# Kernel optimization log

Measured on AMD Instinct MI355X. Metric: run time of the kernel, lower is better.

Reference implementation:

```python
import jax, jax.numpy as jnp
import numpy as np
import math

N = 100000
E = 1600000
D_IN = 128
H = 128
OUT = 10
NEG = -1e30


def setup_inputs() -> dict:
    key = jax.random.key(0)
    ks = jax.random.split(key, 24)
    def lin(k, fi, fo):
        s = 1.0 / np.sqrt(fi)
        return jax.random.uniform(k, (fi, fo), jnp.float32, -s, s)
    inp = {
        'x': jax.random.normal(ks[0], (N, D_IN), jnp.float32),
        'edge_index': jax.random.randint(ks[1], (2, E), 0, N, jnp.int64),
        'W1': lin(ks[2], D_IN, H), 'b1': jnp.zeros((H,), jnp.float32),
        'ws1': lin(ks[3], H, 1), 'bs1': jnp.zeros((1,), jnp.float32),
        'W2': lin(ks[4], H, H), 'b2': jnp.zeros((H,), jnp.float32),
        'ws2': lin(ks[5], H, 1), 'bs2': jnp.zeros((1,), jnp.float32),
        'W3': lin(ks[6], H, H), 'b3': jnp.zeros((H,), jnp.float32),
        'ws3': lin(ks[7], H, 1), 'bs3': jnp.zeros((1,), jnp.float32),
        'M1': lin(ks[8], 2 * H, H), 'bm1': jnp.zeros((H,), jnp.float32),
        'M2': lin(ks[9], H, H // 2), 'bm2': jnp.zeros((H // 2,), jnp.float32),
        'M3': lin(ks[10], H // 2, OUT), 'bm3': jnp.zeros((OUT,), jnp.float32),
    }
    return inp


def _gcn(x, W, b, src, dst, node_mask, edge_mask):
    # GCNConv with self-loops: deg[i] = self_loop + in_degree over valid edges
    deg = node_mask + jax.ops.segment_sum(edge_mask, dst, num_segments=N)
    dinv = jnp.where(deg > 0, jax.lax.rsqrt(deg), 0.0)
    coef = edge_mask * dinv[src] * dinv[dst]            # [E]
    agg = jax.ops.segment_sum(coef[:, None] * x[src], dst, num_segments=N)
    agg = agg + (node_mask * dinv * dinv)[:, None] * x   # self-loop term
    return (agg @ W + b) * node_mask[:, None]


def _sag_pool(x, ws, bs, src, dst, node_mask, edge_mask, k):
    # score via 1-dim GCNConv, top-k (ratio 0.5) select, tanh gating, edge filtering
    score = _gcn(x, ws, bs, src, dst, node_mask, edge_mask)[:, 0]
    _, idx = jax.lax.top_k(jnp.where(node_mask > 0, score, -jnp.inf), k)
    new_mask = jnp.zeros((N,), x.dtype).at[idx].set(1.0)
    x_new = x * jnp.tanh(score)[:, None] * new_mask[:, None]
    e_new = edge_mask * new_mask[src] * new_mask[dst]
    return x_new, new_mask, e_new


def _readout(x, mask, k):
    mean = jnp.sum(x * mask[:, None], axis=0) / k
    mx = jnp.max(jnp.where(mask[:, None] > 0, x, NEG), axis=0)
    return jnp.concatenate([mean, mx])[None, :]   # [1, 2H]


def reference(x, edge_index, W1, b1, ws1, bs1, W2, b2, ws2, bs2, W3, b3, ws3, bs3, M1, bm1, M2, bm2, M3, bm3):
    src, dst = edge_index[0], edge_index[1]
    nm0 = jnp.ones((N,), jnp.float32)
    em0 = jnp.ones((E,), jnp.float32)
    k1 = math.ceil(0.5 * N)
    k2 = math.ceil(0.5 * k1)
    k3 = math.ceil(0.5 * k2)

    h1 = jax.nn.relu(_gcn(x, W1, b1, src, dst, nm0, em0))
    x1, nm1, em1 = _sag_pool(h1, ws1, bs1, src, dst, nm0, em0, k1)
    r1 = _readout(x1, nm1, k1)

    h2 = jax.nn.relu(_gcn(x1, W2, b2, src, dst, nm1, em1))
    x2, nm2, em2 = _sag_pool(h2, ws2, bs2, src, dst, nm1, em1, k2)
    r2 = _readout(x2, nm2, k2)

    h3 = jax.nn.relu(_gcn(x2, W3, b3, src, dst, nm2, em2))
    x3, nm3, em3 = _sag_pool(h3, ws3, bs3, src, dst, nm2, em2, k3)
    r3 = _readout(x3, nm3, k3)

    readout = r1 + r2 + r3                              # [1, 2H]
    y = jax.nn.relu(readout @ M1 + bm1)
    y = jax.nn.relu(y @ M2 + bm2)
    y = y @ M3 + bm3
    return jax.nn.log_softmax(y, axis=1)
```

## Files before the change

### kernel.cpp

```cpp
#include <hip/hip_runtime.h>
#include <cstdint>
#include <cstddef>

#define NN 100000
#define EE 1600000
#define HH 128
#define NB_N 391
#define NBKT 391
#define CAP 5120
#define NCH 16
#define SPC 25


typedef float f32x2 __attribute__((ext_vector_type(2)));
typedef float f32x4 __attribute__((ext_vector_type(4)));
typedef short bf16x8 __attribute__((ext_vector_type(8)));

static __device__ __forceinline__ unsigned fsort_(float f){
  unsigned u = __float_as_uint(f);
  return (u & 0x80000000u) ? ~u : (u | 0x80000000u);
}
static __device__ __forceinline__ unsigned bfbits_(float f){
  unsigned u = __float_as_uint(f);
  return (u + 0x7FFFu + ((u >> 16) & 1u)) >> 16;
}
static __device__ __forceinline__ unsigned bfpack_(float f0, float f1){
  return bfbits_(f0) | (bfbits_(f1) << 16);
}
static __device__ __forceinline__ float bflo_(unsigned u){ return __uint_as_float(u << 16); }
static __device__ __forceinline__ float bfhi_(unsigned u){ return __uint_as_float(u & 0xFFFF0000u); }

__global__ void k_init(const int* __restrict__ ei, unsigned* __restrict__ state,
                       unsigned* __restrict__ bktcnt,
                       const float* __restrict__ W0, const float* __restrict__ W1,
                       const float* __restrict__ W2,
                       unsigned short* __restrict__ WtH, unsigned short* __restrict__ WtL){
  int t = threadIdx.x;
  if(blockIdx.x == 3){
    if(t < 64){
      int v = ei[2*t + 1];
      unsigned long long m = __ballot(v != 0);
      if(t == 0) state[8] = (m == 0ull) ? 1u : 0u;
    }
    if(t >= 12 && t < 24) state[t] = 0u;
    for(int j=t; j<NBKT; j+=256) bktcnt[j] = 0u;
  } else {
    int m = blockIdx.x;
    const float* W = (m==0)?W0:((m==1)?W1:W2);
    unsigned short* th = WtH + m*16384;
    unsigned short* tl = WtL + m*16384;
    for(int i=t; i<16384; i+=256){
      int k = i & 127, n = i >> 7;
      float w = W[k*128 + n];
      unsigned hb = bfbits_(w);
      float hf = __uint_as_float(hb<<16);
      unsigned lb = bfbits_(w - hf);
      th[n*128 + k] = (unsigned short)hb;
      tl[n*128 + k] = (unsigned short)lb;
    }
  }
}

__global__ __launch_bounds__(256) void k_binA(const int* __restrict__ ei,
                     const unsigned* __restrict__ state,
                     unsigned* __restrict__ bktcnt, unsigned* __restrict__ staging){
  __shared__ unsigned lcnt[NBKT];
  __shared__ unsigned gbase[NBKT];
  __shared__ unsigned lloc[NBKT];
  __shared__ unsigned pfx[512];
  __shared__ unsigned sortv[4096];
  __shared__ unsigned short bktid[4096];
  int t = threadIdx.x;
  for(int j=t; j<NBKT; j+=256){ lcnt[j] = 0u; lloc[j] = 0u; }
  bool i64 = (state[8] != 0u);
  int e0 = blockIdx.x*4096;
  int es[16], ed[16];
  #pragma unroll
  for(int k=0;k<16;k++){
    int e = e0 + k*256 + t;
    int s = -1, d = 0;
    if(e < EE){
      if(i64){ s = ei[2*e]; d = ei[2*EE + 2*e]; }
      else   { s = ei[e];   d = ei[EE + e]; }
    }
    es[k] = s; ed[k] = d;
  }
  __syncthreads();
  #pragma unroll
  for(int k=0;k<16;k++){
    if(es[k] >= 0) atomicAdd(&lcnt[ed[k]>>8], 1u);
  }
  __syncthreads();
  int j0 = t, j1 = t + 256;
  pfx[j0] = (j0 < NBKT) ? lcnt[j0] : 0u;
  pfx[j1] = (j1 < NBKT) ? lcnt[j1] : 0u;
  __syncthreads();
  for(int off=1; off<512; off<<=1){
    unsigned u0 = (j0 >= off) ? pfx[j0-off] : 0u;
    unsigned u1 = (j1 >= off) ? pfx[j1-off] : 0u;
    __syncthreads();
    pfx[j0] += u0;
    pfx[j1] += u1;
    __syncthreads();
  }
  unsigned total = pfx[NBKT-1];
  for(int j=t; j<NBKT; j+=256){
    unsigned c = lcnt[j];
    gbase[j] = c ? atomicAdd(&bktcnt[j], c) : 0u;
  }
  __syncthreads();
  #pragma unroll
  for(int k=0;k<16;k++){
    if(es[k] >= 0){
      int b = ed[k] >> 8;
      unsigned slot = (pfx[b] - lcnt[b]) + atomicAdd(&lloc[b], 1u);
      sortv[slot] = (unsigned)es[k] | (((unsigned)(ed[k] & 255)) << 17);
      bktid[slot] = (unsigned short)b;
    }
  }
  __syncthreads();
  for(unsigned i=t; i<total; i+=256){
    unsigned b = bktid[i];
    unsigned local = i - (pfx[b] - lcnt[b]);
    unsigned off = gbase[b] + local;
    if(off < CAP) staging[b*CAP + off] = sortv[i];
  }
}

__global__ __launch_bounds__(256) void k_binB(const unsigned* __restrict__ staging,
                     const unsigned* __restrict__ bktcnt,
                     int* __restrict__ rs, int* __restrict__ rl, int* __restrict__ col,
                     float* __restrict__ dinv){
  __shared__ unsigned hist[256];
  __shared__ unsigned pref[256];
  __shared__ unsigned lfill[256];
  __shared__ unsigned baseSh;
  __shared__ int colsh[CAP];
  int t = threadIdx.x;
  int b = blockIdx.x;
  unsigned s = 0;
  for(int j=t; j<b; j+=256) s += bktcnt[j];
  pref[t] = s;
  __syncthreads();
  for(int off=128; off>0; off>>=1){
    if(t < off) pref[t] += pref[t+off];
    __syncthreads();
  }
  if(t == 0) baseSh = pref[0];
  __syncthreads();
  unsigned base = baseSh;
  unsigned cnt = bktcnt[b]; if(cnt > CAP) cnt = CAP;
  hist[t] = 0u; lfill[t] = 0u;
  __syncthreads();
  const unsigned* st = staging + (unsigned)b*CAP;
  for(unsigned i=t; i<cnt; i+=256) atomicAdd(&hist[st[i]>>17], 1u);
  __syncthreads();
  unsigned h = hist[t];
  pref[t] = h;
  __syncthreads();
  for(int off=1; off<256; off<<=1){
    unsigned u = (t >= off) ? pref[t-off] : 0u;
    __syncthreads();
    pref[t] += u;
    __syncthreads();
  }
  unsigned excl = pref[t] - h;
  int node = b*256 + t;
  if(node < NN){
    rs[node] = (int)(base + excl);
    rl[node] = (int)h;
    dinv[node] = rsqrtf(1.f + (float)h);
  }
  __syncthreads();
  pref[t] = excl;
  __syncthreads();
  for(unsigned i=t; i<cnt; i+=256){
    unsigned w = st[i];
    unsigned dl = w >> 17;
    unsigned pos = pref[dl] + atomicAdd(&lfill[dl], 1u);
    colsh[pos] = (int)(w & 0x1FFFFu);
  }
  __syncthreads();
  for(unsigned i=t; i<cnt; i+=256) col[base+i] = colsh[i];
}

template<int MODE>
__global__ __launch_bounds__(256) void k_gemmM(const void* __restrict__ xin_,
        const float* __restrict__ gate, const float* __restrict__ dinv,
        const int* __restrict__ alist, int nrows,
        const unsigned short* __restrict__ WtH, const unsigned short* __restrict__ WtL,
        unsigned short* __restrict__ y16){
  __shared__ __attribute__((aligned(16))) unsigned short sWh[128*128];
  __shared__ __attribute__((aligned(16))) unsigned short sWl[128*128];
  __shared__ __attribute__((aligned(16))) unsigned short sB[4][16*128];
  int t = threadIdx.x;
  for(int f = t; f < 2048; f += 256){
    int colw = f >> 4, kc = f & 15;
    uint4 vh = *(const uint4*)(WtH + colw*128 + kc*8);
    uint4 vl = *(const uint4*)(WtL + colw*128 + kc*8);
    int dst = colw*128 + ((kc ^ (colw & 15)) << 3);
    *(uint4*)&sWh[dst] = vh;
    *(uint4*)&sWl[dst] = vl;
  }
  int lane = t & 63, wid = t >> 6;
  int lg = lane >> 4, lc = lane & 15;
  int rb = blockIdx.x*64 + wid*16;
  int arow = rb + lc;
  int anode = 0;
  if(arow < nrows) anode = MODE ? alist[arow] : arow;
  bf16x8 a_h[4], a_l[4];
  if(MODE){
    const unsigned short* xp = (const unsigned short*)xin_ + (size_t)anode*HH + lg*8;
    #pragma unroll
    for(int kw=0;kw<4;kw++) a_h[kw] = *(const bf16x8*)(xp + kw*32);
  } else {
    const float* xp = (const float*)xin_ + (size_t)anode*HH + lg*8;
    #pragma unroll
    for(int kw=0;kw<4;kw++){
      float4 x0 = *(const float4*)(xp + kw*32);
      float4 x1 = *(const float4*)(xp + kw*32 + 4);
      float xs[8] = {x0.x,x0.y,x0.z,x0.w,x1.x,x1.y,x1.z,x1.w};
      #pragma unroll
      for(int e=0;e<8;e++){
        unsigned hb = bfbits_(xs[e]);
        float hf = __uint_as_float(hb<<16);
        unsigned lb = bfbits_(xs[e]-hf);
        a_h[kw][e] = (short)hb;
        a_l[kw][e] = (short)lb;
      }
    }
  }
  __syncthreads();
  f32x4 acc[8];
  #pragma unroll
  for(int c=0;c<8;c++) acc[c] = (f32x4){0.f,0.f,0.f,0.f};
  #pragma unroll
  for(int kw=0;kw<4;kw++){
    int kch = kw*4 + lg;
    bf16x8 bh[8], bl[8];
    #pragma unroll
    for(int c=0;c<8;c++){
      int idx = (c*16 + lc)*128 + ((kch ^ lc) << 3);
      bh[c] = *(const bf16x8*)&sWh[idx];
      bl[c] = *(const bf16x8*)&sWl[idx];
    }
    #pragma unroll
    for(int c=0;c<8;c++)
      acc[c] = __builtin_amdgcn_mfma_f32_16x16x32_bf16(a_h[kw], bh[c], acc[c], 0,0,0);
    if(MODE){
      #pragma unroll
      for(int c=0;c<8;c++)
        acc[c] = __builtin_amdgcn_mfma_f32_16x16x32_bf16(a_h[kw], bl[c], acc[c], 0,0,0);
    } else {
      #pragma unroll
      for(int c=0;c<8;c++)
        acc[c] = __builtin_amdgcn_mfma_f32_16x16x32_bf16(a_l[kw], bh[c], acc[c], 0,0,0);
      #pragma unroll
      for(int c=0;c<8;c++)
        acc[c] = __builtin_amdgcn_mfma_f32_16x16x32_bf16(a_h[kw], bl[c], acc[c], 0,0,0);
    }
  }
  float s[4];
  #pragma unroll
  for(int r=0;r<4;r++){
    int gr = rb + lg*4 + r;
    float sv = 0.f;
    if(gr < nrows){
      int nd = MODE ? alist[gr] : gr;
      sv = MODE ? dinv[nd]*gate[nd] : dinv[nd];
    }
    s[r] = sv;
  }
  #pragma unroll
  for(int c=0;c<8;c++){
    #pragma unroll
    for(int r=0;r<4;r++)
      sB[wid][(lg*4+r)*128 + c*16 + lc] = (unsigned short)bfbits_(acc[c][r]*s[r]);
  }
  #pragma unroll
  for(int it=0; it<4; it++){
    int row = it*4 + lg;
    int grow = rb + row;
    uint4 v = *(const uint4*)&sB[wid][row*128 + lc*8];
    if(grow < nrows){
      int nd = MODE ? alist[grow] : grow;
      *(uint4*)&y16[(size_t)nd*HH + lc*8] = v;
    }
  }
}

#define ACCQ(V) do{ \
  f32x2 t0,t1,t2,t3; \
  t0.x=__uint_as_float((V).x<<16); t0.y=__uint_as_float((V).x&0xFFFF0000u); \
  t1.x=__uint_as_float((V).y<<16); t1.y=__uint_as_float((V).y&0xFFFF0000u); \
  t2.x=__uint_as_float((V).z<<16); t2.y=__uint_as_float((V).z&0xFFFF0000u); \
  t3.x=__uint_as_float((V).w<<16); t3.y=__uint_as_float((V).w&0xFFFF0000u); \
  a01+=t0; a23+=t1; a45+=t2; a67+=t3; }while(0)

template<int LIST>
__global__ __launch_bounds__(256) void k_agg(const unsigned short* __restrict__ y16,
        const float* __restrict__ dinv,
        const int* __restrict__ rs, const int* __restrict__ rl,
        const int* __restrict__ col, const int* __restrict__ alist,
        const float* __restrict__ bias, const float* __restrict__ wsc,
        unsigned short* __restrict__ h16, float* __restrict__ p,
        unsigned* __restrict__ hist){
  if(blockIdx.x < 512) hist[blockIdx.x*256 + threadIdx.x] = 0u;
  int w = (blockIdx.x*256 + threadIdx.x) >> 6;
  int lane = threadIdx.x & 63;
  int g = lane >> 4, c = lane & 15;
  int node = LIST ? alist[w] : w;
  float di = dinv[node];
  int e0 = rs[node], len = rl[node];
  const char* yb = (const char*)y16;
  unsigned lc16 = (unsigned)(c << 4);
  int chunk = (len + 3) >> 2;
  int ib = g*chunk;
  int ie = ib + chunk; if(ie > len) ie = len;
  f32x2 a01 = {0.f,0.f}, a23 = {0.f,0.f}, a45 = {0.f,0.f}, a67 = {0.f,0.f};
  const int* ce = col + e0;
  int i = ib;
  for(; i+3 < ie; i += 4){
    int c0 = ce[i], c1 = ce[i+1], c2 = ce[i+2], c3 = ce[i+3];
    uint4 v0 = *(const uint4*)(yb + (((unsigned)c0<<8) | lc16));
    uint4 v1 = *(const uint4*)(yb + (((unsigned)c1<<8) | lc16));
    uint4 v2 = *(const uint4*)(yb + (((unsigned)c2<<8) | lc16));
    uint4 v3 = *(const uint4*)(yb + (((unsigned)c3<<8) | lc16));
    ACCQ(v0); ACCQ(v1); ACCQ(v2); ACCQ(v3);
  }
  for(; i < ie; i++){
    int c0 = ce[i];
    uint4 v0 = *(const uint4*)(yb + (((unsigned)c0<<8) | lc16));
    ACCQ(v0);
  }
  float a0=a01.x, a1=a01.y, a2=a23.x, a3=a23.y, a4=a45.x, a5=a45.y, a6=a67.x, a7=a67.y;
  a0 += __shfl_xor(a0,16,64); a0 += __shfl_xor(a0,32,64);
  a1 += __shfl_xor(a1,16,64); a1 += __shfl_xor(a1,32,64);
  a2 += __shfl_xor(a2,16,64); a2 += __shfl_xor(a2,32,64);
  a3 += __shfl_xor(a3,16,64); a3 += __shfl_xor(a3,32,64);
  a4 += __shfl_xor(a4,16,64); a4 += __shfl_xor(a4,32,64);
  a5 += __shfl_xor(a5,16,64); a5 += __shfl_xor(a5,32,64);
  a6 += __shfl_xor(a6,16,64); a6 += __shfl_xor(a6,32,64);
  a7 += __shfl_xor(a7,16,64); a7 += __shfl_xor(a7,32,64);
  uint4 sv = *(const uint4*)(yb + (((unsigned)node<<8) | lc16));
  const float4* b4 = (const float4*)bias;
  float4 bb0 = b4[2*c], bb1 = b4[2*c+1];
  float o0 = fmaxf(fmaf(di, a0 + bflo_(sv.x), bb0.x), 0.f);
  float o1 = fmaxf(fmaf(di, a1 + bfhi_(sv.x), bb0.y), 0.f);
  float o2 = fmaxf(fmaf(di, a2 + bflo_(sv.y), bb0.z), 0.f);
  float o3 = fmaxf(fmaf(di, a3 + bfhi_(sv.y), bb0.w), 0.f);
  float o4 = fmaxf(fmaf(di, a4 + bflo_(sv.z), bb1.x), 0.f);
  float o5 = fmaxf(fmaf(di, a5 + bfhi_(sv.z), bb1.y), 0.f);
  float o6 = fmaxf(fmaf(di, a6 + bflo_(sv.w), bb1.z), 0.f);
  float o7 = fmaxf(fmaf(di, a7 + bfhi_(sv.w), bb1.w), 0.f);
  if(g == 0){
    uint4 o;
    o.x = bfpack_(o0,o1); o.y = bfpack_(o2,o3);
    o.z = bfpack_(o4,o5); o.w = bfpack_(o6,o7);
    ((uint4*)(h16 + (size_t)node*HH))[c] = o;
  }
  const float4* w4 = (const float4*)wsc;
  float4 w0 = w4[2*c], w1 = w4[2*c+1];
  float pp = o0*w0.x + o1*w0.y + o2*w0.z + o3*w0.w
           + o4*w1.x + o5*w1.y + o6*w1.z + o7*w1.w;
  pp += __shfl_xor(pp, 1, 64);
  pp += __shfl_xor(pp, 2, 64);
  pp += __shfl_xor(pp, 4, 64);
  pp += __shfl_xor(pp, 8, 64);
  if(lane == 0) p[node] = di*pp;
}

template<int LIST>
__global__ void k_score(const float* __restrict__ p, const float* __restrict__ dinv,
                        const int* __restrict__ rs, const int* __restrict__ rl,
                        const int* __restrict__ col, const int* __restrict__ alist, int n,
                        const float* __restrict__ bs, float* __restrict__ score,
                        unsigned* __restrict__ key, unsigned* __restrict__ hist){
  int w = blockIdx.x*256 + threadIdx.x;
  if(w >= n) return;
  int i = LIST ? alist[w] : w;
  float di = dinv[i];
  float s = 0.f;
  int e0 = rs[i], len = rl[i];
  const int* ce = col + e0;
  int e = 0;
  for(; e+3 < len; e += 4){
    int c0 = ce[e], c1 = ce[e+1], c2 = ce[e+2], c3 = ce[e+3];
    s += (p[c0] + p[c1]) + (p[c2] + p[c3]);
  }
  for(; e < len; e++) s += p[ce[e]];
  float sc = di*(s + p[i]) + bs[0];
  score[i] = sc;
  unsigned kv = fsort_(sc);
  key[i] = kv;
  atomicAdd(&hist[kv>>16], 1u);
}

__global__ void k_hist_lo(const unsigned* __restrict__ key, const unsigned* __restrict__ state,
                          unsigned* __restrict__ histB){
  int i = blockIdx.x*256 + threadIdx.x;
  if(i < NN){
    unsigned kv = key[i];
    if((kv >> 16) == state[0]) atomicAdd(&histB[kv & 0xFFFFu], 1u);
  }
}
__global__ void k_pick(const unsigned* __restrict__ hist, unsigned* __restrict__ state,
                       int k_in, int mode){
  __shared__ unsigned csum[256];
  int t = threadIdx.x;
  const uint4* h4 = (const uint4*)(hist + t*256);
  unsigned s = 0;
  for(int j=0;j<64;j++){ uint4 v = h4[j]; s += v.x+v.y+v.z+v.w; }
  csum[t] = s;
  __syncthreads();
  for(int off=1; off<256; off<<=1){
    unsigned v = (t+off < 256) ? csum[t+off] : 0u;
    __syncthreads();
    csum[t] += v;
    __syncthreads();
  }
  unsigned k = (mode == 0) ? (unsigned)k_in : state[1];
  unsigned above = csum[t] - s;
  if(above < k && above + s >= k){
    unsigned run = above;
    for(int j=255; j>=0; j--){
      unsigned c = hist[t*256+j];
      if(run + c >= k){
        if(mode == 0){ state[0] = (unsigned)(t*256+j); state[1] = k - run; }
        else { state[2] = (state[0] << 16) | (unsigned)(t*256+j); state[3] = k - run; }
        break;
      }
      run += c;
    }
  }
}

__global__ __launch_bounds__(256) void k_maskCR(unsigned* __restrict__ key,
        const float* __restrict__ score, const unsigned* __restrict__ state,
        const unsigned short* __restrict__ h16,
        unsigned* __restrict__ selb, float* __restrict__ gate,
        int* __restrict__ alist_out, unsigned* __restrict__ acounter,
        float* __restrict__ rpart, int slotbase){
  __shared__ int wcnt[4];
  __shared__ int priorSh;
  __shared__ int redi[256];
  __shared__ float gl[256];
  __shared__ unsigned char slf[256];
  __shared__ float4 red[256];
  __shared__ float out2[256];
  int t = threadIdx.x;
  int i = blockIdx.x*256 + t;
  unsigned T = state[2];
  int trem = (int)state[3];
  unsigned kv = (i < NN) ? key[i] : 0u;
  bool match = (kv == T);
  unsigned long long m = __ballot(match);
  int lane = t & 63, wid = t >> 6;
  if(lane == 0) wcnt[wid] = __popcll(m);
  if(t == 0) priorSh = 0;
  __syncthreads();
  int hasMatch = wcnt[0] | wcnt[1] | wcnt[2] | wcnt[3];
  int bbase = blockIdx.x*256;
  if(hasMatch){
    int cm = 0;
    for(int j = t*4; j < bbase; j += 1024){
      uint4 kk = *(const uint4*)&key[j];
      cm += (kk.x==T) + (kk.y==T) + (kk.z==T) + (kk.w==T);
    }
    redi[t] = cm;
    __syncthreads();
    for(int off=128; off>0; off>>=1){
      if(t < off) redi[t] += redi[t+off];
      __syncthreads();
    }
    if(t == 0) priorSh = redi[0];
    __syncthreads();
  }
  int pre = 0;
  for(int w=0; w<wid; w++) pre += wcnt[w];
  int lrank = __popcll(m & ((1ull << lane) - 1ull));
  int rank = priorSh + pre + lrank;
  bool sel = (kv > T) || (match && rank < trem);
  float gg = sel ? tanhf(score[i]) : 0.f;
  gl[t] = gg;
  slf[t] = sel ? 1 : 0;
  if(i < NN){
    gate[i] = gg;
    if(!sel) key[i] = 0u;
  }
  unsigned long long sm = __ballot(sel);
  if(lane == 0){
    int widx = blockIdx.x*4 + wid;
    selb[widx*2]   = (unsigned)sm;
    selb[widx*2+1] = (unsigned)(sm >> 32);
  }
  unsigned abase = 0;
  if(lane == 0) abase = atomicAdd(acounter, (unsigned)__popcll(sm));
  abase = (unsigned)__shfl((int)abase, 0, 64);
  if(sel) alist_out[abase + __popcll(sm & ((1ull << lane) - 1ull))] = i;
  __syncthreads();
  int ch = t & 15;
  int slot = t >> 4;
  float mm[8] = {0,0,0,0,0,0,0,0};
  float MM[8] = {-1e30f,-1e30f,-1e30f,-1e30f,-1e30f,-1e30f,-1e30f,-1e30f};
  for(int itr=0; itr<16; itr++){
    int nl = slot + itr*16;
    int node = bbase + nl;
    if(node < NN && slf[nl]){
      float g = gl[nl];
      uint4 v = ((const uint4*)(h16 + (size_t)node*HH))[ch];
      float x0 = g*bflo_(v.x), x1 = g*bfhi_(v.x);
      float x2 = g*bflo_(v.y), x3 = g*bfhi_(v.y);
      float x4 = g*bflo_(v.z), x5 = g*bfhi_(v.z);
      float x6 = g*bflo_(v.w), x7 = g*bfhi_(v.w);
      mm[0]+=x0; mm[1]+=x1; mm[2]+=x2; mm[3]+=x3;
      mm[4]+=x4; mm[5]+=x5; mm[6]+=x6; mm[7]+=x7;
      MM[0]=fmaxf(MM[0],x0); MM[1]=fmaxf(MM[1],x1); MM[2]=fmaxf(MM[2],x2); MM[3]=fmaxf(MM[3],x3);
      MM[4]=fmaxf(MM[4],x4); MM[5]=fmaxf(MM[5],x5); MM[6]=fmaxf(MM[6],x6); MM[7]=fmaxf(MM[7],x7);
    }
  }
  #pragma unroll
  for(int half=0; half<2; half++){
    red[t] = make_float4(mm[half*4+0],mm[half*4+1],mm[half*4+2],mm[half*4+3]);
    __syncthreads();
    if(t < 16){
      float4 sacc = red[t];
      for(int j=1;j<16;j++){
        float4 o = red[t + 16*j];
        sacc.x += o.x; sacc.y += o.y; sacc.z += o.z; sacc.w += o.w;
      }
      int d = t*8 + half*4;
      out2[d+0] = sacc.x; out2[d+1] = sacc.y; out2[d+2] = sacc.z; out2[d+3] = sacc.w;
    }
    __syncthreads();
    red[t] = make_float4(MM[half*4+0],MM[half*4+1],MM[half*4+2],MM[half*4+3]);
    __syncthreads();
    if(t < 16){
      float4 sacc = red[t];
      for(int j=1;j<16;j++){
        float4 o = red[t + 16*j];
        sacc.x = fmaxf(sacc.x,o.x); sacc.y = fmaxf(sacc.y,o.y);
        sacc.z = fmaxf(sacc.z,o.z); sacc.w = fmaxf(sacc.w,o.w);
      }
      int d = 128 + t*8 + half*4;
      out2[d+0] = sacc.x; out2[d+1] = sacc.y; out2[d+2] = sacc.z; out2[d+3] = sacc.w;
    }
    __syncthreads();
  }
  rpart[(size_t)(slotbase + blockIdx.x)*256 + t] = out2[t];
}

__global__ __launch_bounds__(256) void k_compact(const int* __restrict__ alist, int n,
        const unsigned* __restrict__ selb,
        const int* __restrict__ rs_old, const int* __restrict__ rl_old,
        const int* __restrict__ col_old,
        int* __restrict__ rs_new, int* __restrict__ rl_new, int* __restrict__ col_new,
        float* __restrict__ dinv, unsigned* __restrict__ ecnt){
  __shared__ unsigned gcnt[16];
  __shared__ unsigned gbase[16];
  __shared__ unsigned blkbase;
  int t = threadIdx.x;
  int g = t >> 4, lane = t & 15;
  int gsh = ((t >> 4) & 3) * 16;
  int idx = blockIdx.x*16 + g;
  int node = -1, e0 = 0, len = 0;
  if(idx < n){ node = alist[idx]; e0 = rs_old[node]; len = rl_old[node]; }
  int cnt = 0;
  for(int i=lane; i<len; i+=16){
    int s = col_old[e0+i];
    cnt += (int)((selb[s>>5] >> (s&31)) & 1u);
  }
  cnt += __shfl_xor(cnt,1,64); cnt += __shfl_xor(cnt,2,64);
  cnt += __shfl_xor(cnt,4,64); cnt += __shfl_xor(cnt,8,64);
  if(lane == 0) gcnt[g] = (node >= 0) ? (unsigned)cnt : 0u;
  __syncthreads();
  if(t == 0){
    unsigned s = 0;
    for(int j=0;j<16;j++){ gbase[j] = s; s += gcnt[j]; }
    blkbase = s ? atomicAdd(ecnt, s) : 0u;
  }
  __syncthreads();
  unsigned base = blkbase + gbase[g];
  if(node >= 0 && lane == 0){
    rs_new[node] = (int)base;
    rl_new[node] = cnt;
    dinv[node] = rsqrtf(1.f + (float)cnt);
  }
  int pos = (int)base;
  for(int i0=0; i0<len; i0+=16){
    int i = i0 + lane;
    bool keep = false; int s = 0;
    if(i < len){ s = col_old[e0+i]; keep = ((selb[s>>5] >> (s&31)) & 1u) != 0u; }
    unsigned long long b = __ballot(keep);
    unsigned gb = (unsigned)((b >> gsh) & 0xFFFFull);
    int rank = __popc(gb & ((1u << lane) - 1u));
    if(keep) col_new[pos + rank] = s;
    pos += __popc(gb);
  }
}

__global__ void k_red(const float* __restrict__ rpart, float* __restrict__ rpart2){
  int l = blockIdx.x >> 4, c = blockIdx.x & 15;
  int t = threadIdx.x;
  int j0 = c*SPC, j1 = j0 + SPC; if(j1 > NB_N) j1 = NB_N;
  const float* rp = rpart + (size_t)l*NB_N*256;
  float r;
  if(t < 128){
    float s0=0.f,s1=0.f,s2=0.f,s3=0.f;
    int j = j0;
    for(; j+3 < j1; j += 4){
      s0 += rp[(size_t)(j  )*256 + t];
      s1 += rp[(size_t)(j+1)*256 + t];
      s2 += rp[(size_t)(j+2)*256 + t];
      s3 += rp[(size_t)(j+3)*256 + t];
    }
    for(; j < j1; j++) s0 += rp[(size_t)j*256 + t];
    r = (s0+s1)+(s2+s3);
  } else {
    float m0=-1e30f,m1=-1e30f,m2=-1e30f,m3=-1e30f;
    int j = j0;
    for(; j+3 < j1; j += 4){
      m0 = fmaxf(m0, rp[(size_t)(j  )*256 + t]);
      m1 = fmaxf(m1, rp[(size_t)(j+1)*256 + t]);
      m2 = fmaxf(m2, rp[(size_t)(j+2)*256 + t]);
      m3 = fmaxf(m3, rp[(size_t)(j+3)*256 + t]);
    }
    for(; j < j1; j++) m0 = fmaxf(m0, rp[(size_t)j*256 + t]);
    r = fmaxf(fmaxf(m0,m1), fmaxf(m2,m3));
  }
  rpart2[(size_t)blockIdx.x*256 + t] = r;
}

__global__ void k_mlp(const float* __restrict__ rpart2,
                      const float* __restrict__ M1, const float* __restrict__ bm1,
                      const float* __restrict__ M2, const float* __restrict__ bm2,
                      const float* __restrict__ M3, const float* __restrict__ bm3,
                      float* __restrict__ out){
  __shared__ float R[256];
  __shared__ float y1[128];
  __shared__ float y2[64];
  __shared__ float y3[16];
  int t = threadIdx.x;
  const float kinv[3] = {1.f/50000.f, 1.f/25000.f, 1.f/12500.f};
  if(t < 128){
    float acc = 0.f;
    for(int l=0; l<3; l++){
      float s = 0.f;
      #pragma unroll
      for(int c=0; c<NCH; c++) s += rpart2[(size_t)(l*NCH+c)*256 + t];
      acc += s * kinv[l];
    }
    R[t] = acc;
  } else {
    float acc = 0.f;
    for(int l=0; l<3; l++){
      float m = -1e30f;
      #pragma unroll
      for(int c=0; c<NCH; c++) m = fmaxf(m, rpart2[(size_t)(l*NCH+c)*256 + t]);
      acc += m;
    }
    R[t] = acc;
  }
  __syncthreads();
  if(t < 128){
    float a = bm1[t];
    for(int d=0; d<256; d++) a += R[d]*M1[d*128+t];
    y1[t] = fmaxf(a, 0.f);
  }
  __syncthreads();
  if(t < 64){
    float a = bm2[t];
    for(int d=0; d<128; d++) a += y1[d]*M2[d*64+t];
    y2[t] = fmaxf(a, 0.f);
  }
  __syncthreads();
  if(t < 10){
    float a = bm3[t];
    for(int d=0; d<64; d++) a += y2[d]*M3[d*10+t];
    y3[t] = a;
  }
  __syncthreads();
  if(t == 0){
    float mx = -1e30f;
    for(int o=0;o<10;o++) mx = fmaxf(mx, y3[o]);
    float s = 0.f;
    for(int o=0;o<10;o++) s += expf(y3[o]-mx);
    float ls = logf(s);
    for(int o=0;o<10;o++) out[o] = y3[o] - mx - ls;
  }
}

extern "C" void kernel_launch(void* const* d_in, const int* in_sizes, int n_in,
                              void* d_out, int out_size, void* d_ws, size_t ws_size,
                              hipStream_t stream){
  (void)in_sizes; (void)n_in; (void)out_size; (void)ws_size;
  const float* x  = (const float*)d_in[0];
  const int*   ei = (const int*)d_in[1];
  const float* W[3]   = {(const float*)d_in[2],  (const float*)d_in[6],  (const float*)d_in[10]};
  const float* bb[3]  = {(const float*)d_in[3],  (const float*)d_in[7],  (const float*)d_in[11]};
  const float* wsc[3] = {(const float*)d_in[4],  (const float*)d_in[8],  (const float*)d_in[12]};
  const float* bsc[3] = {(const float*)d_in[5],  (const float*)d_in[9],  (const float*)d_in[13]};
  const float* M1  = (const float*)d_in[14];
  const float* bm1 = (const float*)d_in[15];
  const float* M2  = (const float*)d_in[16];
  const float* bm2 = (const float*)d_in[17];
  const float* M3  = (const float*)d_in[18];
  const float* bm3 = (const float*)d_in[19];
  float* out = (float*)d_out;

  char* base = (char*)d_ws;
  size_t off = 0;
  auto alloc = [&](size_t bytes)->char*{
    char* ptr = base + off;
    off += (bytes + 511) & ~(size_t)511;
    return ptr;
  };
  unsigned short* y16  = (unsigned short*)alloc((size_t)NN*HH*2);
  unsigned short* h16  = (unsigned short*)alloc((size_t)NN*HH*2);
  int*      col0      = (int*)     alloc((size_t)EE*4);
  int*      col1      = (int*)     alloc((size_t)EE*4);
  int*      col2      = (int*)     alloc((size_t)EE*4);
  unsigned* staging   = (unsigned*)alloc((size_t)NBKT*CAP*4);
  int*      rs0       = (int*)     alloc((size_t)NN*4);
  int*      rl0       = (int*)     alloc((size_t)NN*4);
  int*      rs1       = (int*)     alloc((size_t)NN*4);
  int*      rl1       = (int*)     alloc((size_t)NN*4);
  int*      rs2       = (int*)     alloc((size_t)NN*4);
  int*      rl2       = (int*)     alloc((size_t)NN*4);
  float*    dinv      = (float*)   alloc((size_t)NN*4);
  float*    pbuf      = (float*)   alloc((size_t)NN*4);
  float*    score     = (float*)   alloc((size_t)NN*4);
  float*    gate      = (float*)   alloc((size_t)NN*4);
  unsigned* key       = (unsigned*)alloc((size_t)NN*4);
  unsigned* selb      = (unsigned*)alloc((size_t)3200*4);
  int*      alistA    = (int*)     alloc((size_t)50000*4);
  int*      alistB    = (int*)     alloc((size_t)25000*4);
  unsigned* hist      = (unsigned*)alloc((size_t)2*65536*4);
  unsigned* bktcnt    = (unsigned*)alloc((size_t)(NBKT+1)*4);
  unsigned* state     = (unsigned*)alloc(256);
  float*    rpart     = (float*)   alloc((size_t)3*NB_N*256*4);
  float*    rpart2    = (float*)   alloc((size_t)3*NCH*256*4);
  unsigned short* WtH = (unsigned short*)alloc((size_t)3*16384*2);
  unsigned short* WtL = (unsigned short*)alloc((size_t)3*16384*2);

  k_init<<<4,256,0,stream>>>(ei, state, bktcnt, W[0], W[1], W[2], WtH, WtL);
  k_binA<<<NBKT,256,0,stream>>>(ei, state, bktcnt, staging);
  k_binB<<<NBKT,256,0,stream>>>(staging, bktcnt, rs0, rl0, col0, dinv);

  k_gemmM<0><<<1563,256,0,stream>>>(x, nullptr, dinv, nullptr, NN, WtH, WtL, y16);
  k_agg<0><<<25000,256,0,stream>>>(y16, dinv, rs0, rl0, col0, nullptr, bb[0], wsc[0], h16, pbuf, hist);
  k_score<0><<<NB_N,256,0,stream>>>(pbuf, dinv, rs0, rl0, col0, nullptr, NN, bsc[0], score, key, hist);
  k_pick<<<1,256,0,stream>>>(hist, state, 50000, 0);
  k_hist_lo<<<NB_N,256,0,stream>>>(key, state, hist + 65536);
  k_pick<<<1,256,0,stream>>>(hist + 65536, state, 0, 1);
  k_maskCR<<<NB_N,256,0,stream>>>(key, score, state, h16, selb, gate, alistA, state+12, rpart, 0);
  k_compact<<<3125,256,0,stream>>>(alistA, 50000, selb, rs0, rl0, col0, rs1, rl1, col1, dinv, state+16);

  k_gemmM<1><<<782,256,0,stream>>>(h16, gate, dinv, alistA, 50000, WtH+16384, WtL+16384, y16);
  k_agg<1><<<12500,256,0,stream>>>(y16, dinv, rs1, rl1, col1, alistA, bb[1], wsc[1], h16, pbuf, hist);
  k_score<1><<<196,256,0,stream>>>(pbuf, dinv, rs1, rl1, col1, alistA, 50000, bsc[1], score, key, hist);
  k_pick<<<1,256,0,stream>>>(hist, state, 25000, 0);
  k_hist_lo<<<NB_N,256,0,stream>>>(key, state, hist + 65536);
  k_pick<<<1,256,0,stream>>>(hist + 65536, state, 0, 1);
  k_maskCR<<<NB_N,256,0,stream>>>(key, score, state, h16, selb, gate, alistB, state+13, rpart, NB_N);
  k_compact<<<1563,256,0,stream>>>(alistB, 25000, selb, rs1, rl1, col1, rs2, rl2, col2, dinv, state+17);

  k_gemmM<1><<<391,256,0,stream>>>(h16, gate, dinv, alistB, 25000, WtH+2*16384, WtL+2*16384, y16);
  k_agg<1><<<6250,256,0,stream>>>(y16, dinv, rs2, rl2, col2, alistB, bb[2], wsc[2], h16, pbuf, hist);
  k_score<1><<<98,256,0,stream>>>(pbuf, dinv, rs2, rl2, col2, alistB, 25000, bsc[2], score, key, hist);
  k_pick<<<1,256,0,stream>>>(hist, state, 12500, 0);
  k_hist_lo<<<NB_N,256,0,stream>>>(key, state, hist + 65536);
  k_pick<<<1,256,0,stream>>>(hist + 65536, state, 0, 1);
  k_maskCR<<<NB_N,256,0,stream>>>(key, score, state, h16, selb, gate, alistA, state+14, rpart, 2*NB_N);

  k_red<<<3*NCH,256,0,stream>>>(rpart, rpart2);
  k_mlp<<<1,256,0,stream>>>(rpart2, M1, bm1, M2, bm2, M3, bm3, out);
}
```

Baseline: 686.2 us.

## Split aggregation into feature slabs per block and parallelize top-k bucket pick

The aggregation kernel now gives each block one of 8 feature slabs (16 features) for 16 nodes, so consecutive blocks share the same source rows and gather 8-byte pieces rather than 16-byte ones. The intent is better cache locality for the gathers. Per-slab score partials go to a new p8 buffer and a new k_psum kernel sums them, which adds a launch and some extra traffic. Separately, k_pick replaces its serial 256-step scan over the chosen row with a parallel shared-memory prefix scan.

```diff
diff --git a/kernel.cpp b/kernel.cpp
--- a/kernel.cpp
+++ b/kernel.cpp
@@ -289,85 +289,77 @@
   }
 }
 
-#define ACCQ(V) do{ \
-  f32x2 t0,t1,t2,t3; \
-  t0.x=__uint_as_float((V).x<<16); t0.y=__uint_as_float((V).x&0xFFFF0000u); \
-  t1.x=__uint_as_float((V).y<<16); t1.y=__uint_as_float((V).y&0xFFFF0000u); \
-  t2.x=__uint_as_float((V).z<<16); t2.y=__uint_as_float((V).z&0xFFFF0000u); \
-  t3.x=__uint_as_float((V).w<<16); t3.y=__uint_as_float((V).w&0xFFFF0000u); \
-  a01+=t0; a23+=t1; a45+=t2; a67+=t3; }while(0)
-
 template<int LIST>
 __global__ __launch_bounds__(256) void k_agg(const unsigned short* __restrict__ y16,
         const float* __restrict__ dinv,
         const int* __restrict__ rs, const int* __restrict__ rl,
         const int* __restrict__ col, const int* __restrict__ alist,
         const float* __restrict__ bias, const float* __restrict__ wsc,
-        unsigned short* __restrict__ h16, float* __restrict__ p,
-        unsigned* __restrict__ hist){
+        unsigned short* __restrict__ h16, float* __restrict__ p8,
+        unsigned* __restrict__ hist, int n){
   if(blockIdx.x < 512) hist[blockIdx.x*256 + threadIdx.x] = 0u;
-  int w = (blockIdx.x*256 + threadIdx.x) >> 6;
-  int lane = threadIdx.x & 63;
-  int g = lane >> 4, c = lane & 15;
-  int node = LIST ? alist[w] : w;
-  float di = dinv[node];
-  int e0 = rs[node], len = rl[node];
+  int slab = blockIdx.x & 7;
+  int w = ((blockIdx.x >> 3) << 4) + (threadIdx.x >> 4);
+  int nl = threadIdx.x & 15;
+  int g = nl >> 2, c = nl & 3;
+  bool act = (w < n);
+  int node = 0;
+  if(act) node = LIST ? alist[w] : w;
+  float di = act ? dinv[node] : 0.f;
+  int e0 = 0, len = 0;
+  if(act){ e0 = rs[node]; len = rl[node]; }
   const char* yb = (const char*)y16;
-  unsigned lc16 = (unsigned)(c << 4);
-  int chunk = (len + 3) >> 2;
-  int ib = g*chunk;
-  int ie = ib + chunk; if(ie > len) ie = len;
-  f32x2 a01 = {0.f,0.f}, a23 = {0.f,0.f}, a45 = {0.f,0.f}, a67 = {0.f,0.f};
+  unsigned off8 = ((unsigned)slab << 5) | ((unsigned)c << 3);
+  float a0=0.f, a1=0.f, a2=0.f, a3=0.f;
   const int* ce = col + e0;
-  int i = ib;
-  for(; i+3 < ie; i += 4){
-    int c0 = ce[i], c1 = ce[i+1], c2 = ce[i+2], c3 = ce[i+3];
-    uint4 v0 = *(const uint4*)(yb + (((unsigned)c0<<8) | lc16));
-    uint4 v1 = *(const uint4*)(yb + (((unsigned)c1<<8) | lc16));
-    uint4 v2 = *(const uint4*)(yb + (((unsigned)c2<<8) | lc16));
-    uint4 v3 = *(const uint4*)(yb + (((unsigned)c3<<8) | lc16));
-    ACCQ(v0); ACCQ(v1); ACCQ(v2); ACCQ(v3);
-  }
-  for(; i < ie; i++){
-    int c0 = ce[i];
-    uint4 v0 = *(const uint4*)(yb + (((unsigned)c0<<8) | lc16));
-    ACCQ(v0);
-  }
-  float a0=a01.x, a1=a01.y, a2=a23.x, a3=a23.y, a4=a45.x, a5=a45.y, a6=a67.x, a7=a67.y;
-  a0 += __shfl_xor(a0,16,64); a0 += __shfl_xor(a0,32,64);
-  a1 += __shfl_xor(a1,16,64); a1 += __shfl_xor(a1,32,64);
-  a2 += __shfl_xor(a2,16,64); a2 += __shfl_xor(a2,32,64);
-  a3 += __shfl_xor(a3,16,64); a3 += __shfl_xor(a3,32,64);
-  a4 += __shfl_xor(a4,16,64); a4 += __shfl_xor(a4,32,64);
-  a5 += __shfl_xor(a5,16,64); a5 += __shfl_xor(a5,32,64);
-  a6 += __shfl_xor(a6,16,64); a6 += __shfl_xor(a6,32,64);
-  a7 += __shfl_xor(a7,16,64); a7 += __shfl_xor(a7,32,64);
-  uint4 sv = *(const uint4*)(yb + (((unsigned)node<<8) | lc16));
-  const float4* b4 = (const float4*)bias;
-  float4 bb0 = b4[2*c], bb1 = b4[2*c+1];
-  float o0 = fmaxf(fmaf(di, a0 + bflo_(sv.x), bb0.x), 0.f);
-  float o1 = fmaxf(fmaf(di, a1 + bfhi_(sv.x), bb0.y), 0.f);
-  float o2 = fmaxf(fmaf(di, a2 + bflo_(sv.y), bb0.z), 0.f);
-  float o3 = fmaxf(fmaf(di, a3 + bfhi_(sv.y), bb0.w), 0.f);
-  float o4 = fmaxf(fmaf(di, a4 + bflo_(sv.z), bb1.x), 0.f);
-  float o5 = fmaxf(fmaf(di, a5 + bfhi_(sv.z), bb1.y), 0.f);
-  float o6 = fmaxf(fmaf(di, a6 + bflo_(sv.w), bb1.z), 0.f);
-  float o7 = fmaxf(fmaf(di, a7 + bfhi_(sv.w), bb1.w), 0.f);
-  if(g == 0){
-    uint4 o;
+  int i = g;
+  for(; i + 4 < len; i += 8){
+    int s0 = ce[i], s1 = ce[i+4];
+    uint2 v0 = *(const uint2*)(yb + (((unsigned)s0<<8) | off8));
+    uint2 v1 = *(const uint2*)(yb + (((unsigned)s1<<8) | off8));
+    a0 += bflo_(v0.x) + bflo_(v1.x);
+    a1 += bfhi_(v0.x) + bfhi_(v1.x);
+    a2 += bflo_(v0.y) + bflo_(v1.y);
+    a3 += bfhi_(v0.y) + bfhi_(v1.y);
+  }
+  if(i < len){
+    int s0 = ce[i];
+    uint2 v0 = *(const uint2*)(yb + (((unsigned)s0<<8) | off8));
+    a0 += bflo_(v0.x); a1 += bfhi_(v0.x);
+    a2 += bflo_(v0.y); a3 += bfhi_(v0.y);
+  }
+  a0 += __shfl_xor(a0,4,64); a0 += __shfl_xor(a0,8,64);
+  a1 += __shfl_xor(a1,4,64); a1 += __shfl_xor(a1,8,64);
+  a2 += __shfl_xor(a2,4,64); a2 += __shfl_xor(a2,8,64);
+  a3 += __shfl_xor(a3,4,64); a3 += __shfl_xor(a3,8,64);
+  uint2 sv = make_uint2(0u,0u);
+  if(act) sv = *(const uint2*)(yb + (((unsigned)node<<8) | off8));
+  float4 bb = ((const float4*)bias)[slab*4 + c];
+  float4 wv = ((const float4*)wsc)[slab*4 + c];
+  float o0 = fmaxf(fmaf(di, a0 + bflo_(sv.x), bb.x), 0.f);
+  float o1 = fmaxf(fmaf(di, a1 + bfhi_(sv.x), bb.y), 0.f);
+  float o2 = fmaxf(fmaf(di, a2 + bflo_(sv.y), bb.z), 0.f);
+  float o3 = fmaxf(fmaf(di, a3 + bfhi_(sv.y), bb.w), 0.f);
+  if(g == 0 && act){
+    uint2 o;
     o.x = bfpack_(o0,o1); o.y = bfpack_(o2,o3);
-    o.z = bfpack_(o4,o5); o.w = bfpack_(o6,o7);
-    ((uint4*)(h16 + (size_t)node*HH))[c] = o;
-  }
-  const float4* w4 = (const float4*)wsc;
-  float4 w0 = w4[2*c], w1 = w4[2*c+1];
-  float pp = o0*w0.x + o1*w0.y + o2*w0.z + o3*w0.w
-           + o4*w1.x + o5*w1.y + o6*w1.z + o7*w1.w;
+    *(uint2*)&h16[(size_t)node*HH + slab*16 + c*4] = o;
+  }
+  float pp = o0*wv.x + o1*wv.y + o2*wv.z + o3*wv.w;
   pp += __shfl_xor(pp, 1, 64);
   pp += __shfl_xor(pp, 2, 64);
-  pp += __shfl_xor(pp, 4, 64);
-  pp += __shfl_xor(pp, 8, 64);
-  if(lane == 0) p[node] = di*pp;
+  if(nl == 0 && act) p8[(size_t)node*8 + slab] = di*pp;
+}
+
+template<int LIST>
+__global__ void k_psum(const float* __restrict__ p8, const int* __restrict__ alist, int n,
+                       float* __restrict__ p){
+  int w = blockIdx.x*256 + threadIdx.x;
+  if(w >= n) return;
+  int i = LIST ? alist[w] : w;
+  const float4* q = (const float4*)(p8 + (size_t)i*8);
+  float4 u = q[0], v = q[1];
+  p[i] = ((u.x+u.y)+(u.z+u.w)) + ((v.x+v.y)+(v.z+v.w));
 }
 
 template<int LIST>
@@ -407,11 +399,15 @@
 __global__ void k_pick(const unsigned* __restrict__ hist, unsigned* __restrict__ state,
                        int k_in, int mode){
   __shared__ unsigned csum[256];
+  __shared__ unsigned vrow[256];
+  __shared__ int rowSh;
+  __shared__ unsigned aboveSh;
   int t = threadIdx.x;
   const uint4* h4 = (const uint4*)(hist + t*256);
   unsigned s = 0;
   for(int j=0;j<64;j++){ uint4 v = h4[j]; s += v.x+v.y+v.z+v.w; }
   csum[t] = s;
+  if(t == 0) rowSh = -1;
   __syncthreads();
   for(int off=1; off<256; off<<=1){
     unsigned v = (t+off < 256) ? csum[t+off] : 0u;
@@ -421,16 +417,27 @@
   }
   unsigned k = (mode == 0) ? (unsigned)k_in : state[1];
   unsigned above = csum[t] - s;
-  if(above < k && above + s >= k){
-    unsigned run = above;
-    for(int j=255; j>=0; j--){
-      unsigned c = hist[t*256+j];
-      if(run + c >= k){
-        if(mode == 0){ state[0] = (unsigned)(t*256+j); state[1] = k - run; }
-        else { state[2] = (state[0] << 16) | (unsigned)(t*256+j); state[3] = k - run; }
-        break;
-      }
-      run += c;
+  if(above < k && above + s >= k){ rowSh = t; aboveSh = above; }
+  __syncthreads();
+  int row = rowSh;
+  if(row >= 0){
+    vrow[t] = hist[row*256 + t];
+    __syncthreads();
+    for(int off=1; off<256; off<<=1){
+      unsigned u = (t+off < 256) ? vrow[t+off] : 0u;
+      __syncthreads();
+      vrow[t] += u;
+      __syncthreads();
+    }
+    unsigned above2 = aboveSh;
+    unsigned sincl = vrow[t];
+    unsigned snext = (t < 255) ? vrow[t+1] : 0u;
+    bool cond  = (above2 + sincl >= k);
+    bool condn = (above2 + snext >= k);
+    if(cond && !condn){
+      unsigned run = above2 + snext;
+      if(mode == 0){ state[0] = (unsigned)(row*256+t); state[1] = k - run; }
+      else { state[2] = (state[0] << 16) | (unsigned)(row*256+t); state[3] = k - run; }
     }
   }
 }
@@ -729,6 +736,7 @@
   int*      rl2       = (int*)     alloc((size_t)NN*4);
   float*    dinv      = (float*)   alloc((size_t)NN*4);
   float*    pbuf      = (float*)   alloc((size_t)NN*4);
+  float*    p8        = (float*)   alloc((size_t)NN*8*4);
   float*    score     = (float*)   alloc((size_t)NN*4);
   float*    gate      = (float*)   alloc((size_t)NN*4);
   unsigned* key       = (unsigned*)alloc((size_t)NN*4);
@@ -748,7 +756,8 @@
   k_binB<<<NBKT,256,0,stream>>>(staging, bktcnt, rs0, rl0, col0, dinv);
 
   k_gemmM<0><<<1563,256,0,stream>>>(x, nullptr, dinv, nullptr, NN, WtH, WtL, y16);
-  k_agg<0><<<25000,256,0,stream>>>(y16, dinv, rs0, rl0, col0, nullptr, bb[0], wsc[0], h16, pbuf, hist);
+  k_agg<0><<<50000,256,0,stream>>>(y16, dinv, rs0, rl0, col0, nullptr, bb[0], wsc[0], h16, p8, hist, NN);
+  k_psum<0><<<NB_N,256,0,stream>>>(p8, nullptr, NN, pbuf);
   k_score<0><<<NB_N,256,0,stream>>>(pbuf, dinv, rs0, rl0, col0, nullptr, NN, bsc[0], score, key, hist);
   k_pick<<<1,256,0,stream>>>(hist, state, 50000, 0);
   k_hist_lo<<<NB_N,256,0,stream>>>(key, state, hist + 65536);
@@ -757,7 +766,8 @@
   k_compact<<<3125,256,0,stream>>>(alistA, 50000, selb, rs0, rl0, col0, rs1, rl1, col1, dinv, state+16);
 
   k_gemmM<1><<<782,256,0,stream>>>(h16, gate, dinv, alistA, 50000, WtH+16384, WtL+16384, y16);
-  k_agg<1><<<12500,256,0,stream>>>(y16, dinv, rs1, rl1, col1, alistA, bb[1], wsc[1], h16, pbuf, hist);
+  k_agg<1><<<25000,256,0,stream>>>(y16, dinv, rs1, rl1, col1, alistA, bb[1], wsc[1], h16, p8, hist, 50000);
+  k_psum<1><<<196,256,0,stream>>>(p8, alistA, 50000, pbuf);
   k_score<1><<<196,256,0,stream>>>(pbuf, dinv, rs1, rl1, col1, alistA, 50000, bsc[1], score, key, hist);
   k_pick<<<1,256,0,stream>>>(hist, state, 25000, 0);
   k_hist_lo<<<NB_N,256,0,stream>>>(key, state, hist + 65536);
@@ -766,7 +776,8 @@
   k_compact<<<1563,256,0,stream>>>(alistB, 25000, selb, rs1, rl1, col1, rs2, rl2, col2, dinv, state+17);
 
   k_gemmM<1><<<391,256,0,stream>>>(h16, gate, dinv, alistB, 25000, WtH+2*16384, WtL+2*16384, y16);
-  k_agg<1><<<6250,256,0,stream>>>(y16, dinv, rs2, rl2, col2, alistB, bb[2], wsc[2], h16, pbuf, hist);
+  k_agg<1><<<12504,256,0,stream>>>(y16, dinv, rs2, rl2, col2, alistB, bb[2], wsc[2], h16, p8, hist, 25000);
+  k_psum<1><<<98,256,0,stream>>>(p8, alistB, 25000, pbuf);
   k_score<1><<<98,256,0,stream>>>(pbuf, dinv, rs2, rl2, col2, alistB, 25000, bsc[2], score, key, hist);
   k_pick<<<1,256,0,stream>>>(hist, state, 12500, 0);
   k_hist_lo<<<NB_N,256,0,stream>>>(key, state, hist + 65536);
```

Measured after the change: 825.0 us. 20.2% more time.
